# Kernel optimization log

Hardware: AMD Instinct MI355X
Metric: run time of the kernel (lower is better)

Reference implementation:

```python
import jax, jax.numpy as jnp
import numpy as np

N_NODES = 16384   # n_nodes
N_LINKS = 8192    # batch of target links
D_EMB = 128       # embedding dim
EDGE_P = 0.004    # adjacency density -> avg degree ~65


def setup_inputs() -> dict:
    key = jax.random.key(0)
    k1, k2, k3 = jax.random.split(key, 3)
    adj = jax.random.bernoulli(k1, EDGE_P, (N_NODES, N_NODES))
    adj = adj | adj.T                      # symmetric graph
    adj = adj & ~jnp.eye(N_NODES, dtype=bool)  # no self loops
    links = jax.random.randint(k2, (N_LINKS, 2), 0, N_NODES)
    emb = jax.random.normal(k3, (N_NODES, D_EMB), dtype=jnp.float32)
    return {"targetLink": links, "adjacent": adj, "NodeEmbedding": emb}


def reference(targetLink, adjacent, NodeEmbedding):
    # targetLink: [B,2] int, adjacent: [N,N] bool, NodeEmbedding: [N,D] float
    i = targetLink[:, 0]
    j = targetLink[:, 1]
    emb_i = NodeEmbedding[i]               # [B,D] gather
    emb_j = NodeEmbedding[j]               # [B,D] gather
    product = emb_i * emb_j                # [B,D]
    # common-neighbor indicator: u is a CN of (i,j) iff adj[i,u] and adj[j,u]
    cn_mask = (adjacent[i] & adjacent[j]).astype(NodeEmbedding.dtype)  # [B,N]
    # sum of embeddings over common neighbors (fused gather-reduce)
    cn_sum = cn_mask @ NodeEmbedding       # [B,D]
    return jnp.concatenate([product, cn_sum], axis=-1)  # [B,2D]
```

## Files before the change

kernel.cpp:

```cpp
#include <hip/hip_runtime.h>

#define N_NODES 16384
#define D_EMB   128
#define LIST_CAP 1024
#define BM_WORDS 512
#define BM_U64   256
#define FLAG_OFF N_NODES
#define BM_OFF_BYTES (1 << 17)
#define WS_NEEDED (BM_OFF_BYTES + (size_t)N_NODES * (BM_WORDS * 4))

__global__ __launch_bounds__(256) void zero_probe_kernel(
    const unsigned int* __restrict__ words, int* __restrict__ flags)
{
    const int idx = blockIdx.x * 256 + threadIdx.x;
    flags[idx] = 0;
    if (blockIdx.x == 0) {
        __shared__ int s_any;
        if (threadIdx.x == 0) s_any = 0;
        __syncthreads();
        int any = 0;
        for (int k = threadIdx.x; k < 16384; k += 256)
            if (words[k] > 1u) any = 1;
        if (any) atomicOr(&s_any, 1);
        __syncthreads();
        if (threadIdx.x == 0) flags[FLAG_OFF] = s_any;
    }
}

__global__ __launch_bounds__(256) void mark_kernel(
    const int* __restrict__ links, int* __restrict__ flags, int n_endpoints)
{
    const int k = blockIdx.x * 256 + threadIdx.x;
    if (k < n_endpoints) flags[links[k]] = 1;
}

__global__ __launch_bounds__(256) void compress_pack_kernel(
    const unsigned int* __restrict__ adj, const int* __restrict__ flags,
    unsigned long long* __restrict__ bm64)
{
    const int r = blockIdx.x;
    if (flags[FLAG_OFF] != 0) return;
    if (!flags[r]) return;

    const int t = threadIdx.x;
    const uint4* row = reinterpret_cast<const uint4*>(adj + (size_t)r * N_NODES);

    unsigned int lo = 0u, hi = 0u;
#pragma unroll
    for (int k = 0; k < 8; ++k) {
        const uint4 v = row[k * 256 + t];
        const unsigned int nib = min(v.x, 1u) | (min(v.y, 1u) << 1)
                               | (min(v.z, 1u) << 2) | (min(v.w, 1u) << 3);
        lo |= nib << (4 * k);
    }
#pragma unroll
    for (int k = 8; k < 16; ++k) {
        const uint4 v = row[k * 256 + t];
        const unsigned int nib = min(v.x, 1u) | (min(v.y, 1u) << 1)
                               | (min(v.z, 1u) << 2) | (min(v.w, 1u) << 3);
        hi |= nib << (4 * (k - 8));
    }
    bm64[(size_t)r * BM_U64 + t] = ((unsigned long long)hi << 32) | lo;
}

__global__ __launch_bounds__(256) void compress_byte_kernel(
    const unsigned char* __restrict__ adj, const int* __restrict__ flags,
    unsigned int* __restrict__ bm)
{
    const int r = blockIdx.x;
    if (flags[FLAG_OFF] == 0) return;
    if (!flags[r]) return;
    unsigned int* dst = bm + (size_t)r * BM_WORDS;
    const int t = threadIdx.x;
    __shared__ unsigned int s_nib[256];

    const uint4* row = reinterpret_cast<const uint4*>(adj + (size_t)r * N_NODES);
#pragma unroll
    for (int c = 0; c < 4; ++c) {
        const uint4 v = row[c * 256 + t];
        const unsigned int arr[4] = {v.x, v.y, v.z, v.w};
        unsigned int half = 0;
#pragma unroll
        for (int a = 0; a < 4; ++a)
#pragma unroll
            for (int bb = 0; bb < 4; ++bb)
                half |= ((((arr[a] >> (8 * bb)) & 0xFFu) ? 1u : 0u) << (a * 4 + bb));
        s_nib[t] = half;
        __syncthreads();
        if (t < 128)
            dst[c * 128 + t] = s_nib[t * 2] | (s_nib[t * 2 + 1] << 16);
        __syncthreads();
    }
}

__global__ __launch_bounds__(256) void link_kernel(
    const int* __restrict__ links, const unsigned long long* __restrict__ bm64,
    const float* __restrict__ emb, float* __restrict__ out,
    const int* __restrict__ flags, int n_links)
{
    const int link = blockIdx.x;
    if (link >= n_links) return;
    const int i = links[2 * link];
    const int j = links[2 * link + 1];
    const int byte_layout = flags[FLAG_OFF];

    __shared__ int s_list[LIST_CAP];
    __shared__ int s_count;
    if (threadIdx.x == 0) s_count = 0;
    __syncthreads();

    const int t = threadIdx.x;
    unsigned long long m = bm64[(size_t)i * BM_U64 + t]
                         & bm64[(size_t)j * BM_U64 + t];
    while (m) {
        const int b = __ffsll(m) - 1;
        m &= m - 1;
        const int node = byte_layout
            ? (t * 64 + b)
            : (((b >> 5) << 13) + (((b & 31) >> 2) << 10) + (t << 2) + (b & 3));
        const int pos = atomicAdd(&s_count, 1);
        if (pos < LIST_CAP) s_list[pos] = node;
    }
    __syncthreads();

    int count = s_count;
    if (count > LIST_CAP) count = LIST_CAP;

    const size_t obase = (size_t)link * (2 * D_EMB);
    if (t < D_EMB) {
        out[obase + t] = emb[(size_t)i * D_EMB + t] * emb[(size_t)j * D_EMB + t];
    } else {
        const int d = t - D_EMB;
        float s = 0.0f;
        for (int c = 0; c < count; ++c)
            s += emb[(size_t)s_list[c] * D_EMB + d];
        out[obase + D_EMB + d] = s;
    }
}

__global__ __launch_bounds__(256) void detect_layout_kernel(
    const unsigned int* __restrict__ words, int* __restrict__ flag)
{
    __shared__ int s_any;
    if (threadIdx.x == 0) s_any = 0;
    __syncthreads();
    int any = 0;
    for (int k = threadIdx.x; k < 16384; k += 256)
        if (words[k] > 1u) any = 1;
    if (any) atomicOr(&s_any, 1);
    __syncthreads();
    if (threadIdx.x == 0) *flag = s_any;
}

__global__ __launch_bounds__(256) void ncn_direct(
    const int* __restrict__ links, const void* __restrict__ adjv,
    const float* __restrict__ emb, float* __restrict__ out,
    const int* __restrict__ flag, int n_links)
{
    const int link = blockIdx.x;
    if (link >= n_links) return;
    const int i = links[2 * link];
    const int j = links[2 * link + 1];

    __shared__ int s_list[LIST_CAP];
    __shared__ int s_count;
    if (threadIdx.x == 0) s_count = 0;
    __syncthreads();

    const int byte_layout = flag ? flag[0] : 0;
    if (byte_layout) {
        const uint4* rowi = reinterpret_cast<const uint4*>(
            (const unsigned char*)adjv + (size_t)i * N_NODES);
        const uint4* rowj = reinterpret_cast<const uint4*>(
            (const unsigned char*)adjv + (size_t)j * N_NODES);
#pragma unroll
        for (int c = 0; c < 4; ++c) {
            const int idx = c * 256 + threadIdx.x;
            const uint4 a = rowi[idx];
            const uint4 b = rowj[idx];
            unsigned int m[4] = {a.x & b.x, a.y & b.y, a.z & b.z, a.w & b.w};
            if (m[0] | m[1] | m[2] | m[3]) {
                const int base = idx * 16;
#pragma unroll
                for (int w = 0; w < 4; ++w) {
                    unsigned int v = m[w];
                    if (!v) continue;
#pragma unroll
                    for (int b8 = 0; b8 < 4; ++b8) {
                        if ((v >> (8 * b8)) & 0xFFu) {
                            int pos = atomicAdd(&s_count, 1);
                            if (pos < LIST_CAP) s_list[pos] = base + w * 4 + b8;
                        }
                    }
                }
            }
        }
    } else {
        const uint4* rowi = reinterpret_cast<const uint4*>(
            (const int*)adjv + (size_t)i * N_NODES);
        const uint4* rowj = reinterpret_cast<const uint4*>(
            (const int*)adjv + (size_t)j * N_NODES);
#pragma unroll
        for (int c = 0; c < 16; ++c) {
            const int idx = c * 256 + threadIdx.x;
            const uint4 a = rowi[idx];
            const uint4 b = rowj[idx];
            const int base = idx * 4;
            if (a.x & b.x) { int p = atomicAdd(&s_count, 1); if (p < LIST_CAP) s_list[p] = base + 0; }
            if (a.y & b.y) { int p = atomicAdd(&s_count, 1); if (p < LIST_CAP) s_list[p] = base + 1; }
            if (a.z & b.z) { int p = atomicAdd(&s_count, 1); if (p < LIST_CAP) s_list[p] = base + 2; }
            if (a.w & b.w) { int p = atomicAdd(&s_count, 1); if (p < LIST_CAP) s_list[p] = base + 3; }
        }
    }
    __syncthreads();

    int count = s_count;
    if (count > LIST_CAP) count = LIST_CAP;

    const int t = threadIdx.x;
    const size_t obase = (size_t)link * (2 * D_EMB);
    if (t < D_EMB) {
        out[obase + t] = emb[(size_t)i * D_EMB + t] * emb[(size_t)j * D_EMB + t];
    } else {
        const int d = t - D_EMB;
        float s = 0.0f;
        for (int c = 0; c < count; ++c)
            s += emb[(size_t)s_list[c] * D_EMB + d];
        out[obase + D_EMB + d] = s;
    }
}

extern "C" void kernel_launch(void* const* d_in, const int* in_sizes, int n_in,
                              void* d_out, int out_size, void* d_ws, size_t ws_size,
                              hipStream_t stream) {
    const int* links = (const int*)d_in[0];
    const void* adj = d_in[1];
    const float* emb = (const float*)d_in[2];
    float* out = (float*)d_out;

    const int n_links = in_sizes[0] / 2;

    if (ws_size >= WS_NEEDED) {
        int* flags = (int*)d_ws;
        unsigned long long* bm64 =
            (unsigned long long*)((char*)d_ws + BM_OFF_BYTES);
        zero_probe_kernel<<<N_NODES / 256, 256, 0, stream>>>(
            (const unsigned int*)adj, flags);
        mark_kernel<<<(2 * n_links + 255) / 256, 256, 0, stream>>>(
            links, flags, 2 * n_links);
        compress_pack_kernel<<<N_NODES, 256, 0, stream>>>(
            (const unsigned int*)adj, flags, bm64);
        compress_byte_kernel<<<N_NODES, 256, 0, stream>>>(
            (const unsigned char*)adj, flags, (unsigned int*)bm64);
        link_kernel<<<n_links, 256, 0, stream>>>(
            links, bm64, emb, out, flags, n_links);
    } else {
        int* flag = (ws_size >= sizeof(int)) ? (int*)d_ws : nullptr;
        if (flag) detect_layout_kernel<<<1, 256, 0, stream>>>(
            (const unsigned int*)adj, flag);
        ncn_direct<<<n_links, 256, 0, stream>>>(links, adj, emb, out, flag, n_links);
    }
}
```

Before: 176.1 us.

## Fuse five-kernel pipeline into one cooperative persistent kernel with grid syncs

After: 530.4 us. 201% more time.

```diff
diff --git a/kernel.cpp b/kernel.cpp
--- a/kernel.cpp
+++ b/kernel.cpp
@@ -1,140 +1,129 @@
 #include <hip/hip_runtime.h>
+#include <hip/hip_cooperative_groups.h>
+
+namespace cg = cooperative_groups;
 
 #define N_NODES 16384
 #define D_EMB   128
 #define LIST_CAP 1024
-#define BM_WORDS 512
 #define BM_U64   256
 #define FLAG_OFF N_NODES
 #define BM_OFF_BYTES (1 << 17)
-#define WS_NEEDED (BM_OFF_BYTES + (size_t)N_NODES * (BM_WORDS * 4))
-
-__global__ __launch_bounds__(256) void zero_probe_kernel(
-    const unsigned int* __restrict__ words, int* __restrict__ flags)
+#define WS_NEEDED (BM_OFF_BYTES + (size_t)N_NODES * (BM_U64 * 8))
+#define NBLOCKS 1024
+
+__global__ __launch_bounds__(256, 4) void ncn_fused(
+    const int* __restrict__ links,
+    const void* __restrict__ adjv,
+    const float* __restrict__ emb,
+    float* __restrict__ out,
+    int* __restrict__ flags,
+    unsigned long long* __restrict__ bm64,
+    int n_links)
 {
-    const int idx = blockIdx.x * 256 + threadIdx.x;
-    flags[idx] = 0;
-    if (blockIdx.x == 0) {
-        __shared__ int s_any;
-        if (threadIdx.x == 0) s_any = 0;
-        __syncthreads();
+    cg::grid_group grid = cg::this_grid();
+    const int t = threadIdx.x;
+    const int b = blockIdx.x;
+    const int gtid = b * 256 + t;
+
+    if (gtid < N_NODES) flags[gtid] = 0;
+    if (b == 0) {
+        if (t == 0) flags[FLAG_OFF] = 0;
+        __syncthreads();
+        const unsigned int* words = (const unsigned int*)adjv;
         int any = 0;
-        for (int k = threadIdx.x; k < 16384; k += 256)
+        for (int k = t; k < 16384; k += 256)
             if (words[k] > 1u) any = 1;
-        if (any) atomicOr(&s_any, 1);
-        __syncthreads();
-        if (threadIdx.x == 0) flags[FLAG_OFF] = s_any;
-    }
-}
-
-__global__ __launch_bounds__(256) void mark_kernel(
-    const int* __restrict__ links, int* __restrict__ flags, int n_endpoints)
-{
-    const int k = blockIdx.x * 256 + threadIdx.x;
-    if (k < n_endpoints) flags[links[k]] = 1;
-}
-
-__global__ __launch_bounds__(256) void compress_pack_kernel(
-    const unsigned int* __restrict__ adj, const int* __restrict__ flags,
-    unsigned long long* __restrict__ bm64)
-{
-    const int r = blockIdx.x;
-    if (flags[FLAG_OFF] != 0) return;
-    if (!flags[r]) return;
-
-    const int t = threadIdx.x;
-    const uint4* row = reinterpret_cast<const uint4*>(adj + (size_t)r * N_NODES);
-
-    unsigned int lo = 0u, hi = 0u;
-#pragma unroll
-    for (int k = 0; k < 8; ++k) {
-        const uint4 v = row[k * 256 + t];
-        const unsigned int nib = min(v.x, 1u) | (min(v.y, 1u) << 1)
-                               | (min(v.z, 1u) << 2) | (min(v.w, 1u) << 3);
-        lo |= nib << (4 * k);
-    }
-#pragma unroll
-    for (int k = 8; k < 16; ++k) {
-        const uint4 v = row[k * 256 + t];
-        const unsigned int nib = min(v.x, 1u) | (min(v.y, 1u) << 1)
-                               | (min(v.z, 1u) << 2) | (min(v.w, 1u) << 3);
-        hi |= nib << (4 * (k - 8));
-    }
-    bm64[(size_t)r * BM_U64 + t] = ((unsigned long long)hi << 32) | lo;
-}
-
-__global__ __launch_bounds__(256) void compress_byte_kernel(
-    const unsigned char* __restrict__ adj, const int* __restrict__ flags,
-    unsigned int* __restrict__ bm)
-{
-    const int r = blockIdx.x;
-    if (flags[FLAG_OFF] == 0) return;
-    if (!flags[r]) return;
-    unsigned int* dst = bm + (size_t)r * BM_WORDS;
-    const int t = threadIdx.x;
-    __shared__ unsigned int s_nib[256];
-
-    const uint4* row = reinterpret_cast<const uint4*>(adj + (size_t)r * N_NODES);
-#pragma unroll
-    for (int c = 0; c < 4; ++c) {
-        const uint4 v = row[c * 256 + t];
-        const unsigned int arr[4] = {v.x, v.y, v.z, v.w};
-        unsigned int half = 0;
-#pragma unroll
-        for (int a = 0; a < 4; ++a)
-#pragma unroll
-            for (int bb = 0; bb < 4; ++bb)
-                half |= ((((arr[a] >> (8 * bb)) & 0xFFu) ? 1u : 0u) << (a * 4 + bb));
-        s_nib[t] = half;
-        __syncthreads();
-        if (t < 128)
-            dst[c * 128 + t] = s_nib[t * 2] | (s_nib[t * 2 + 1] << 16);
-        __syncthreads();
-    }
-}
-
-__global__ __launch_bounds__(256) void link_kernel(
-    const int* __restrict__ links, const unsigned long long* __restrict__ bm64,
-    const float* __restrict__ emb, float* __restrict__ out,
-    const int* __restrict__ flags, int n_links)
-{
-    const int link = blockIdx.x;
-    if (link >= n_links) return;
-    const int i = links[2 * link];
-    const int j = links[2 * link + 1];
+        if (any) atomicOr(&flags[FLAG_OFF], 1);
+    }
+    grid.sync();
+
+    if (gtid < 2 * n_links) flags[links[gtid]] = 1;
+    grid.sync();
+
     const int byte_layout = flags[FLAG_OFF];
+    if (!byte_layout) {
+        for (int r = b; r < N_NODES; r += NBLOCKS) {
+            if (!flags[r]) continue;
+            const uint4* row = reinterpret_cast<const uint4*>(
+                (const int*)adjv + (size_t)r * N_NODES);
+            unsigned int lo = 0u, hi = 0u;
+#pragma unroll
+            for (int k = 0; k < 8; ++k) {
+                const uint4 v = row[k * 256 + t];
+                const unsigned int nib = min(v.x, 1u) | (min(v.y, 1u) << 1)
+                                       | (min(v.z, 1u) << 2) | (min(v.w, 1u) << 3);
+                lo |= nib << (4 * k);
+            }
+#pragma unroll
+            for (int k = 8; k < 16; ++k) {
+                const uint4 v = row[k * 256 + t];
+                const unsigned int nib = min(v.x, 1u) | (min(v.y, 1u) << 1)
+                                       | (min(v.z, 1u) << 2) | (min(v.w, 1u) << 3);
+                hi |= nib << (4 * (k - 8));
+            }
+            bm64[(size_t)r * BM_U64 + t] = ((unsigned long long)hi << 32) | lo;
+        }
+    } else {
+        for (int r = b; r < N_NODES; r += NBLOCKS) {
+            if (!flags[r]) continue;
+            const uint4* row = reinterpret_cast<const uint4*>(
+                (const unsigned char*)adjv + (size_t)r * N_NODES);
+            unsigned long long bits = 0ull;
+#pragma unroll
+            for (int q = 0; q < 4; ++q) {
+                const uint4 v = row[t * 4 + q];
+                const unsigned int arr[4] = {v.x, v.y, v.z, v.w};
+#pragma unroll
+                for (int a = 0; a < 4; ++a)
+#pragma unroll
+                    for (int bb = 0; bb < 4; ++bb)
+                        if ((arr[a] >> (8 * bb)) & 0xFFu)
+                            bits |= 1ull << (q * 16 + a * 4 + bb);
+            }
+            bm64[(size_t)r * BM_U64 + t] = bits;
+        }
+    }
+    grid.sync();
 
     __shared__ int s_list[LIST_CAP];
     __shared__ int s_count;
-    if (threadIdx.x == 0) s_count = 0;
-    __syncthreads();
-
-    const int t = threadIdx.x;
-    unsigned long long m = bm64[(size_t)i * BM_U64 + t]
-                         & bm64[(size_t)j * BM_U64 + t];
-    while (m) {
-        const int b = __ffsll(m) - 1;
-        m &= m - 1;
-        const int node = byte_layout
-            ? (t * 64 + b)
-            : (((b >> 5) << 13) + (((b & 31) >> 2) << 10) + (t << 2) + (b & 3));
-        const int pos = atomicAdd(&s_count, 1);
-        if (pos < LIST_CAP) s_list[pos] = node;
-    }
-    __syncthreads();
-
-    int count = s_count;
-    if (count > LIST_CAP) count = LIST_CAP;
-
-    const size_t obase = (size_t)link * (2 * D_EMB);
-    if (t < D_EMB) {
-        out[obase + t] = emb[(size_t)i * D_EMB + t] * emb[(size_t)j * D_EMB + t];
-    } else {
-        const int d = t - D_EMB;
-        float s = 0.0f;
-        for (int c = 0; c < count; ++c)
-            s += emb[(size_t)s_list[c] * D_EMB + d];
-        out[obase + D_EMB + d] = s;
+
+    for (int link = b; link < n_links; link += NBLOCKS) {
+        const int i = links[2 * link];
+        const int j = links[2 * link + 1];
+
+        __syncthreads();
+        if (t == 0) s_count = 0;
+        __syncthreads();
+
+        unsigned long long m = bm64[(size_t)i * BM_U64 + t]
+                             & bm64[(size_t)j * BM_U64 + t];
+        while (m) {
+            const int bit = __ffsll(m) - 1;
+            m &= m - 1;
+            const int node = byte_layout
+                ? (t * 64 + bit)
+                : (((bit >> 2) << 10) + (t << 2) + (bit & 3));
+            const int pos = atomicAdd(&s_count, 1);
+            if (pos < LIST_CAP) s_list[pos] = node;
+        }
+        __syncthreads();
+
+        int count = s_count;
+        if (count > LIST_CAP) count = LIST_CAP;
+
+        const size_t obase = (size_t)link * (2 * D_EMB);
+        if (t < D_EMB) {
+            out[obase + t] = emb[(size_t)i * D_EMB + t]
+                           * emb[(size_t)j * D_EMB + t];
+        } else {
+            const int d = t - D_EMB;
+            float s = 0.0f;
+            for (int c = 0; c < count; ++c)
+                s += emb[(size_t)s_list[c] * D_EMB + d];
+            out[obase + D_EMB + d] = s;
+        }
     }
 }
 
@@ -177,8 +166,8 @@
         for (int c = 0; c < 4; ++c) {
             const int idx = c * 256 + threadIdx.x;
             const uint4 a = rowi[idx];
-            const uint4 b = rowj[idx];
-            unsigned int m[4] = {a.x & b.x, a.y & b.y, a.z & b.z, a.w & b.w};
+            const uint4 bq = rowj[idx];
+            unsigned int m[4] = {a.x & bq.x, a.y & bq.y, a.z & bq.z, a.w & bq.w};
             if (m[0] | m[1] | m[2] | m[3]) {
                 const int base = idx * 16;
 #pragma unroll
@@ -204,12 +193,12 @@
         for (int c = 0; c < 16; ++c) {
             const int idx = c * 256 + threadIdx.x;
             const uint4 a = rowi[idx];
-            const uint4 b = rowj[idx];
+            const uint4 bq = rowj[idx];
             const int base = idx * 4;
-            if (a.x & b.x) { int p = atomicAdd(&s_count, 1); if (p < LIST_CAP) s_list[p] = base + 0; }
-            if (a.y & b.y) { int p = atomicAdd(&s_count, 1); if (p < LIST_CAP) s_list[p] = base + 1; }
-            if (a.z & b.z) { int p = atomicAdd(&s_count, 1); if (p < LIST_CAP) s_list[p] = base + 2; }
-            if (a.w & b.w) { int p = atomicAdd(&s_count, 1); if (p < LIST_CAP) s_list[p] = base + 3; }
+            if (a.x & bq.x) { int p = atomicAdd(&s_count, 1); if (p < LIST_CAP) s_list[p] = base + 0; }
+            if (a.y & bq.y) { int p = atomicAdd(&s_count, 1); if (p < LIST_CAP) s_list[p] = base + 1; }
+            if (a.z & bq.z) { int p = atomicAdd(&s_count, 1); if (p < LIST_CAP) s_list[p] = base + 2; }
+            if (a.w & bq.w) { int p = atomicAdd(&s_count, 1); if (p < LIST_CAP) s_list[p] = base + 3; }
         }
     }
     __syncthreads();
@@ -244,16 +233,14 @@
         int* flags = (int*)d_ws;
         unsigned long long* bm64 =
             (unsigned long long*)((char*)d_ws + BM_OFF_BYTES);
-        zero_probe_kernel<<<N_NODES / 256, 256, 0, stream>>>(
-            (const unsigned int*)adj, flags);
-        mark_kernel<<<(2 * n_links + 255) / 256, 256, 0, stream>>>(
-            links, flags, 2 * n_links);
-        compress_pack_kernel<<<N_NODES, 256, 0, stream>>>(
-            (const unsigned int*)adj, flags, bm64);
-        compress_byte_kernel<<<N_NODES, 256, 0, stream>>>(
-            (const unsigned char*)adj, flags, (unsigned int*)bm64);
-        link_kernel<<<n_links, 256, 0, stream>>>(
-            links, bm64, emb, out, flags, n_links);
+
+        void* args[] = {
+            (void*)&links, (void*)&adj, (void*)&emb, (void*)&out,
+            (void*)&flags, (void*)&bm64, (void*)&n_links
+        };
+        hipLaunchCooperativeKernel((const void*)ncn_fused,
+                                   dim3(NBLOCKS), dim3(256),
+                                   args, 0, stream);
     } else {
         int* flag = (ws_size >= sizeof(int)) ? (int*)d_ws : nullptr;
         if (flag) detect_layout_kernel<<<1, 256, 0, stream>>>(
```
